# Kernel optimization log

Hardware: AMD Instinct MI355X
Metric: run time of the kernel (lower is better)

## Reference

```python
import jax, jax.numpy as jnp
import numpy as np

B, IN, OUT, FAN = 2048, 4096, 4096, 64

def setup_inputs() -> dict:
    key = jax.random.key(0)
    k1, k2, k3, k4 = jax.random.split(key, 4)
    input = jax.random.normal(k1, (B, IN), dtype=jnp.float32)
    condensed_weight = jax.random.normal(k2, (OUT, FAN), dtype=jnp.float32) * 0.05
    bias = jax.random.normal(k3, (OUT,), dtype=jnp.float32) * 0.05
    input_mask = jax.random.randint(k4, (OUT, FAN), 0, IN, dtype=jnp.int64)
    return {"input": input, "condensed_weight": condensed_weight,
            "bias": bias, "input_mask": input_mask}

def reference(input, condensed_weight, bias, input_mask):
    # Per output neuron o: sum_f input[b, idx[o,f]] * w[o,f] + bias[o]
    # gathered: [B, OUT, FAN] -- the structured-sparse gather
    gathered = jnp.take(input, input_mask, axis=1)
    return jnp.einsum("bof,of->bo", gathered, condensed_weight) + bias
```

## Files before the change

kernel.cpp:

```cpp
#include <hip/hip_runtime.h>

#define B_DIM   2048
#define IN_DIM  4096
#define OUT_DIM 4096
#define FAN     64


typedef float v2f __attribute__((ext_vector_type(2)));

__device__ __forceinline__ unsigned bf16_rne(float f) {
    unsigned u = __float_as_uint(f);
    return (u + 0x7fffu + ((u >> 16) & 1u)) >> 16;
}

__global__ __launch_bounds__(256) void pack_kernel(
    const float* __restrict__ input, uint4* __restrict__ wsp)
{
    const int idx = blockIdx.x * 256 + threadIdx.x;
    const int t   = idx >> 11;
    const int c0  = (idx & 2047) << 1;

    const float* p = input + (size_t)t * 8 * IN_DIM + c0;
    const float2 r0 = *reinterpret_cast<const float2*>(p + 0 * IN_DIM);
    const float2 r1 = *reinterpret_cast<const float2*>(p + 1 * IN_DIM);
    const float2 r2 = *reinterpret_cast<const float2*>(p + 2 * IN_DIM);
    const float2 r3 = *reinterpret_cast<const float2*>(p + 3 * IN_DIM);
    const float2 r4 = *reinterpret_cast<const float2*>(p + 4 * IN_DIM);
    const float2 r5 = *reinterpret_cast<const float2*>(p + 5 * IN_DIM);
    const float2 r6 = *reinterpret_cast<const float2*>(p + 6 * IN_DIM);
    const float2 r7 = *reinterpret_cast<const float2*>(p + 7 * IN_DIM);

    uint4 a, b;
    a.x = bf16_rne(r0.x) | (bf16_rne(r1.x) << 16);
    a.y = bf16_rne(r2.x) | (bf16_rne(r3.x) << 16);
    a.z = bf16_rne(r4.x) | (bf16_rne(r5.x) << 16);
    a.w = bf16_rne(r6.x) | (bf16_rne(r7.x) << 16);
    b.x = bf16_rne(r0.y) | (bf16_rne(r1.y) << 16);
    b.y = bf16_rne(r2.y) | (bf16_rne(r3.y) << 16);
    b.z = bf16_rne(r4.y) | (bf16_rne(r5.y) << 16);
    b.w = bf16_rne(r6.y) | (bf16_rne(r7.y) << 16);

    uint4* q = wsp + (size_t)t * IN_DIM + c0;
    q[0] = a;
    q[1] = b;
}

template <unsigned BASE>
__device__ __forceinline__ void gather_tile(
    const char* ldsb, const unsigned* paddr, const float* wv,
    float bv, float* op)
{
    v2f a01 = {0.f, 0.f}, a23 = {0.f, 0.f}, a45 = {0.f, 0.f}, a67 = {0.f, 0.f};
    #pragma unroll
    for (int jj = 0; jj < FAN / 2; ++jj) {
        const unsigned pa = paddr[jj];
        const uint4 g0 = *reinterpret_cast<const uint4*>(ldsb + BASE + (pa & 0xffffu));
        const uint4 g1 = *reinterpret_cast<const uint4*>(ldsb + BASE + (pa >> 16));
        {
            const v2f w2 = {wv[2*jj+0], wv[2*jj+0]};
            v2f v;
            v.x = __uint_as_float(g0.x << 16);
            v.y = __uint_as_float(g0.x & 0xffff0000u);
            a01 = __builtin_elementwise_fma(v, w2, a01);
            v.x = __uint_as_float(g0.y << 16);
            v.y = __uint_as_float(g0.y & 0xffff0000u);
            a23 = __builtin_elementwise_fma(v, w2, a23);
            v.x = __uint_as_float(g0.z << 16);
            v.y = __uint_as_float(g0.z & 0xffff0000u);
            a45 = __builtin_elementwise_fma(v, w2, a45);
            v.x = __uint_as_float(g0.w << 16);
            v.y = __uint_as_float(g0.w & 0xffff0000u);
            a67 = __builtin_elementwise_fma(v, w2, a67);
        }
        {
            const v2f w2 = {wv[2*jj+1], wv[2*jj+1]};
            v2f v;
            v.x = __uint_as_float(g1.x << 16);
            v.y = __uint_as_float(g1.x & 0xffff0000u);
            a01 = __builtin_elementwise_fma(v, w2, a01);
            v.x = __uint_as_float(g1.y << 16);
            v.y = __uint_as_float(g1.y & 0xffff0000u);
            a23 = __builtin_elementwise_fma(v, w2, a23);
            v.x = __uint_as_float(g1.z << 16);
            v.y = __uint_as_float(g1.z & 0xffff0000u);
            a45 = __builtin_elementwise_fma(v, w2, a45);
            v.x = __uint_as_float(g1.w << 16);
            v.y = __uint_as_float(g1.w & 0xffff0000u);
            a67 = __builtin_elementwise_fma(v, w2, a67);
        }
    }
    op[0 * OUT_DIM] = a01.x + bv;
    op[1 * OUT_DIM] = a01.y + bv;
    op[2 * OUT_DIM] = a23.x + bv;
    op[3 * OUT_DIM] = a23.y + bv;
    op[4 * OUT_DIM] = a45.x + bv;
    op[5 * OUT_DIM] = a45.y + bv;
    op[6 * OUT_DIM] = a67.x + bv;
    op[7 * OUT_DIM] = a67.y + bv;
}

__device__ __forceinline__ void dma_tile(const uint4* __restrict__ wsp,
                                         uint4* lds, int tile, int tid, int buf)
{
    const uint4* src = wsp + (size_t)tile * IN_DIM + tid;
    uint4*       dst = lds + buf * IN_DIM + tid;
    #pragma unroll
    for (int it = 0; it < 8; ++it) {
        __builtin_amdgcn_global_load_lds(
            (const __attribute__((address_space(1))) unsigned*)(src + it * 512),
            (__attribute__((address_space(3))) unsigned*)(dst + it * 512),
            16, 0, 0);
    }
}

__global__ __launch_bounds__(512, 1) void condensed_kernel(
    const uint4* __restrict__ wsp,
    const float* __restrict__ weight,
    const float* __restrict__ bias,
    const int*   __restrict__ mask,
    float*       __restrict__ out)
{
    extern __shared__ __align__(16) uint4 lds[];

    const int tid   = threadIdx.x;
    const int o     = blockIdx.y * 512 + tid;
    const int bseg  = blockIdx.x * 64;
    const int tbase = bseg >> 3;

    unsigned paddr[FAN / 2];
    float    wv[FAN];
    {
        const int4*   mv = reinterpret_cast<const int4*>(mask)     + o * (FAN / 4);
        const float4* wp = reinterpret_cast<const float4*>(weight) + o * (FAN / 4);
        #pragma unroll
        for (int j = 0; j < FAN / 4; ++j) {
            int4   m4 = mv[j];
            float4 w4 = wp[j];
            paddr[2*j+0] = ((unsigned)m4.x << 4) | ((unsigned)m4.y << 20);
            paddr[2*j+1] = ((unsigned)m4.z << 4) | ((unsigned)m4.w << 20);
            wv[4*j+0] = w4.x;
            wv[4*j+1] = w4.y;
            wv[4*j+2] = w4.z;
            wv[4*j+3] = w4.w;
        }
    }
    const float bv = bias[o];
    const char* ldsb = reinterpret_cast<const char*>(lds);

    dma_tile(wsp, lds, tbase, tid, 0);
    __syncthreads();

    for (int hp = 0; hp < 4; ++hp) {
        const int t0 = hp * 2;

        dma_tile(wsp, lds, tbase + t0 + 1, tid, 1);
        gather_tile<0u>(ldsb, paddr, wv, bv,
                        out + (size_t)(bseg + 8 * t0) * OUT_DIM + o);
        __syncthreads();

        if (hp < 3) {
            dma_tile(wsp, lds, tbase + t0 + 2, tid, 0);
        }
        gather_tile<65536u>(ldsb, paddr, wv, bv,
                            out + (size_t)(bseg + 8 * t0 + 8) * OUT_DIM + o);
        __syncthreads();
    }
}

extern "C" void kernel_launch(void* const* d_in, const int* in_sizes, int n_in,
                              void* d_out, int out_size, void* d_ws, size_t ws_size,
                              hipStream_t stream) {
    const float* input  = (const float*)d_in[0];
    const float* weight = (const float*)d_in[1];
    const float* bias   = (const float*)d_in[2];
    const int*   mask   = (const int*)d_in[3];
    float*       out    = (float*)d_out;
    uint4*       wsp    = (uint4*)d_ws;

    pack_kernel<<<2048, 256, 0, stream>>>(input, wsp);

    hipFuncSetAttribute(reinterpret_cast<const void*>(condensed_kernel),
                        hipFuncAttributeMaxDynamicSharedMemorySize, 131072);
    dim3 grid(32, 8);
    condensed_kernel<<<grid, 512, 131072, stream>>>(wsp, weight, bias, mask, out);
}
```

Measured before the change: 133.1 us.

## Pack bf16 weights with LDS offsets and reorder gathers by bank group

Each per-thread (index, weight) pair is packed into one 32-bit item, with the LDS byte offset in the low half and the weight rounded to bf16 in the high half. This removes the separate fp32 weight array and frees registers. The items are then sorted by LDS bank group (offset bits 4-6) through a per-thread scratch area in LDS, and each thread starts at a rotation given by its lane phase, so neighbouring lanes tend to hit different banks on the same iteration and ds_read_b128 conflicts drop. The cost is a one-time counting sort, an extra barrier, and lower weight precision, which could change accuracy.

Result: slower. 145.1 us (+9.0%).

```diff
diff --git a/kernel.cpp b/kernel.cpp
--- a/kernel.cpp
+++ b/kernel.cpp
@@ -47,17 +47,18 @@
 
 template <unsigned BASE>
 __device__ __forceinline__ void gather_tile(
-    const char* ldsb, const unsigned* paddr, const float* wv,
-    float bv, float* op)
+    const char* ldsb, const unsigned* items, float bv, float* op)
 {
     v2f a01 = {0.f, 0.f}, a23 = {0.f, 0.f}, a45 = {0.f, 0.f}, a67 = {0.f, 0.f};
     #pragma unroll
     for (int jj = 0; jj < FAN / 2; ++jj) {
-        const unsigned pa = paddr[jj];
-        const uint4 g0 = *reinterpret_cast<const uint4*>(ldsb + BASE + (pa & 0xffffu));
-        const uint4 g1 = *reinterpret_cast<const uint4*>(ldsb + BASE + (pa >> 16));
+        const unsigned it0 = items[2*jj+0];
+        const unsigned it1 = items[2*jj+1];
+        const uint4 g0 = *reinterpret_cast<const uint4*>(ldsb + BASE + (it0 & 0xffffu));
+        const uint4 g1 = *reinterpret_cast<const uint4*>(ldsb + BASE + (it1 & 0xffffu));
         {
-            const v2f w2 = {wv[2*jj+0], wv[2*jj+0]};
+            const float wf = __uint_as_float(it0 & 0xffff0000u);
+            const v2f w2 = {wf, wf};
             v2f v;
             v.x = __uint_as_float(g0.x << 16);
             v.y = __uint_as_float(g0.x & 0xffff0000u);
@@ -73,7 +74,8 @@
             a67 = __builtin_elementwise_fma(v, w2, a67);
         }
         {
-            const v2f w2 = {wv[2*jj+1], wv[2*jj+1]};
+            const float wf = __uint_as_float(it1 & 0xffff0000u);
+            const v2f w2 = {wf, wf};
             v2f v;
             v.x = __uint_as_float(g1.x << 16);
             v.y = __uint_as_float(g1.x & 0xffff0000u);
@@ -113,6 +115,9 @@
     }
 }
 
+#define SCRATCH_STRIDE 264
+#define SMEM_BYTES     (512 * SCRATCH_STRIDE > 131072 ? 512 * SCRATCH_STRIDE : 131072)
+
 __global__ __launch_bounds__(512, 1) void condensed_kernel(
     const uint4* __restrict__ wsp,
     const float* __restrict__ weight,
@@ -120,31 +125,71 @@
     const int*   __restrict__ mask,
     float*       __restrict__ out)
 {
-    extern __shared__ __align__(16) uint4 lds[];
+    extern __shared__ __align__(16) unsigned char smem[];
+    uint4* lds = reinterpret_cast<uint4*>(smem);
 
     const int tid   = threadIdx.x;
     const int o     = blockIdx.y * 512 + tid;
     const int bseg  = blockIdx.x * 64;
     const int tbase = bseg >> 3;
 
-    unsigned paddr[FAN / 2];
-    float    wv[FAN];
+    unsigned items[FAN];
     {
+        unsigned raw[FAN];
         const int4*   mv = reinterpret_cast<const int4*>(mask)     + o * (FAN / 4);
         const float4* wp = reinterpret_cast<const float4*>(weight) + o * (FAN / 4);
         #pragma unroll
         for (int j = 0; j < FAN / 4; ++j) {
             int4   m4 = mv[j];
             float4 w4 = wp[j];
-            paddr[2*j+0] = ((unsigned)m4.x << 4) | ((unsigned)m4.y << 20);
-            paddr[2*j+1] = ((unsigned)m4.z << 4) | ((unsigned)m4.w << 20);
-            wv[4*j+0] = w4.x;
-            wv[4*j+1] = w4.y;
-            wv[4*j+2] = w4.z;
-            wv[4*j+3] = w4.w;
+            raw[4*j+0] = ((unsigned)m4.x << 4) | (bf16_rne(w4.x) << 16);
+            raw[4*j+1] = ((unsigned)m4.y << 4) | (bf16_rne(w4.y) << 16);
+            raw[4*j+2] = ((unsigned)m4.z << 4) | (bf16_rne(w4.z) << 16);
+            raw[4*j+3] = ((unsigned)m4.w << 4) | (bf16_rne(w4.w) << 16);
+        }
+
+        int c[8] = {0,0,0,0,0,0,0,0};
+        #pragma unroll
+        for (int k = 0; k < FAN; ++k) {
+            const unsigned g = (raw[k] >> 4) & 7u;
+            #pragma unroll
+            for (int gg = 0; gg < 8; ++gg) c[gg] += (g == (unsigned)gg);
+        }
+        int off[8];
+        off[0] = 0;
+        #pragma unroll
+        for (int g = 1; g < 8; ++g) off[g] = off[g-1] + c[g-1];
+
+        const int ph = tid & 7;
+        int s = 0;
+        #pragma unroll
+        for (int g = 0; g < 8; ++g) s = (ph == g) ? off[g] : s;
+
+        unsigned char* scratch = smem + tid * SCRATCH_STRIDE;
+        int r[8] = {0,0,0,0,0,0,0,0};
+        #pragma unroll
+        for (int k = 0; k < FAN; ++k) {
+            const unsigned g = (raw[k] >> 4) & 7u;
+            int p = 0;
+            #pragma unroll
+            for (int gg = 0; gg < 8; ++gg) {
+                const int m = (g == (unsigned)gg);
+                p = m ? (off[gg] + r[gg]) : p;
+                r[gg] += m;
+            }
+            const int pos = (p - s) & 63;
+            *reinterpret_cast<unsigned*>(scratch + pos * 4) = raw[k];
+        }
+        #pragma unroll
+        for (int k = 0; k < FAN / 2; ++k) {
+            const uint2 t = *reinterpret_cast<const uint2*>(scratch + k * 8);
+            items[2*k+0] = t.x;
+            items[2*k+1] = t.y;
         }
     }
     const float bv = bias[o];
+    __syncthreads();
+
     const char* ldsb = reinterpret_cast<const char*>(lds);
 
     dma_tile(wsp, lds, tbase, tid, 0);
@@ -154,14 +199,14 @@
         const int t0 = hp * 2;
 
         dma_tile(wsp, lds, tbase + t0 + 1, tid, 1);
-        gather_tile<0u>(ldsb, paddr, wv, bv,
+        gather_tile<0u>(ldsb, items, bv,
                         out + (size_t)(bseg + 8 * t0) * OUT_DIM + o);
         __syncthreads();
 
         if (hp < 3) {
             dma_tile(wsp, lds, tbase + t0 + 2, tid, 0);
         }
-        gather_tile<65536u>(ldsb, paddr, wv, bv,
+        gather_tile<65536u>(ldsb, items, bv,
                             out + (size_t)(bseg + 8 * t0 + 8) * OUT_DIM + o);
         __syncthreads();
     }
@@ -180,7 +225,7 @@
     pack_kernel<<<2048, 256, 0, stream>>>(input, wsp);
 
     hipFuncSetAttribute(reinterpret_cast<const void*>(condensed_kernel),
-                        hipFuncAttributeMaxDynamicSharedMemorySize, 131072);
+                        hipFuncAttributeMaxDynamicSharedMemorySize, SMEM_BYTES);
     dim3 grid(32, 8);
-    condensed_kernel<<<grid, 512, 131072, stream>>>(wsp, weight, bias, mask, out);
-}
+    condensed_kernel<<<grid, 512, SMEM_BYTES, stream>>>(wsp, weight, bias, mask, out);
+}
```
